# Kernel optimization log

Hardware: AMD Instinct MI355X
Metric: run time of the kernel (lower is better)

The kernel has to match this reference:

```python
import math
import jax, jax.numpy as jnp
import numpy as np

SIZE = 512
N_HEADS = 8
HEAD = SIZE // N_HEADS
SCALE = 1.0 / math.sqrt(HEAD)


def setup_inputs() -> dict:
    key = jax.random.key(0)
    ks = jax.random.split(key, 10)
    B, Sq, Skv = 4, 2048, 2048
    std = 1.0 / math.sqrt(SIZE)
    inp = {
        "query": jax.random.normal(ks[0], (B, Sq, SIZE), jnp.float32),
        "key_value": jax.random.normal(ks[1], (B, Skv, SIZE), jnp.float32),
        "Wq": jax.random.normal(ks[2], (SIZE, SIZE), jnp.float32) * std,
        "bq": jax.random.normal(ks[3], (SIZE,), jnp.float32) * std,
        "Wk": jax.random.normal(ks[4], (SIZE, SIZE), jnp.float32) * std,
        "bk": jax.random.normal(ks[5], (SIZE,), jnp.float32) * std,
        "Wv": jax.random.normal(ks[6], (SIZE, SIZE), jnp.float32) * std,
        "bv": jax.random.normal(ks[7], (SIZE,), jnp.float32) * std,
        "Wo": jax.random.normal(ks[8], (SIZE, SIZE), jnp.float32) * std,
        "bo": jax.random.normal(ks[9], (SIZE,), jnp.float32) * std,
    }
    return inp


def reference(query, key_value, Wq, bq, Wk, bk, Wv, bv, Wo, bo):
    B, Sq, D = query.shape
    Skv = key_value.shape[1]
    H, hd = N_HEADS, HEAD

    # Linear projections (torch nn.Linear: x @ W.T + b)
    q = query @ Wq.T + bq            # [B, Sq, D]
    k = key_value @ Wk.T + bk        # [B, Skv, D]
    v = key_value @ Wv.T + bv        # [B, Skv, D]

    # split heads: [B, S, H, hd]
    qh = q.reshape(B, Sq, H, hd)
    kh = k.reshape(B, Skv, H, hd)
    vh = v.reshape(B, Skv, H, hd)

    # attention scores and softmax over keys
    scores = jnp.einsum("bqhd,bkhd->bhqk", qh, kh) * SCALE  # [B, H, Sq, Skv]
    A = jax.nn.softmax(scores, axis=-1)
    o = jnp.einsum("bhqk,bkhd->bqhd", A, vh)                 # [B, Sq, H, hd]

    # residual with q heads (clean_path=False), merge heads
    out = (qh + o).reshape(B, Sq, D)

    # output residual + ReLU FFN stage
    out = out + jax.nn.relu(out @ Wo.T + bo)
    return out
```

## Files before the change

kernel.cpp:

```cpp
#include <hip/hip_runtime.h>
#include <hip/hip_bf16.h>

typedef __hip_bfloat16 bf16;
typedef __attribute__((ext_vector_type(4))) float f32x4;
typedef __attribute__((ext_vector_type(16))) float f32x16;
typedef __attribute__((ext_vector_type(8))) __bf16 bf16x8;

#define DEVI static __device__ __forceinline__

DEVI void gload_lds16(const void* g, void* l) {
  __builtin_amdgcn_global_load_lds(
      (const __attribute__((address_space(1))) void*)g,
      (__attribute__((address_space(3))) void*)l, 16, 0, 0);
}

DEVI unsigned pkbf(float a, float b) {
  union { __hip_bfloat162 h2; unsigned u; } t;
  t.h2.x = __float2bfloat16(a);
  t.h2.y = __float2bfloat16(b);
  return t.u;
}

union PK4 { bf16 h[4]; unsigned long long ll; };

DEVI unsigned long long pack4(float4 v) {
  PK4 u;
  u.h[0] = __float2bfloat16(v.x); u.h[1] = __float2bfloat16(v.y);
  u.h[2] = __float2bfloat16(v.z); u.h[3] = __float2bfloat16(v.w);
  return u.ll;
}

__global__ void cvt_all(const float* __restrict__ q, const float* __restrict__ kv,
                        const float* __restrict__ wq, const float* __restrict__ wk,
                        const float* __restrict__ wv, const float* __restrict__ wo,
                        bf16* __restrict__ oq, bf16* __restrict__ okv,
                        bf16* __restrict__ owq, bf16* __restrict__ owk,
                        bf16* __restrict__ owv, bf16* __restrict__ owo) {
  int bid = blockIdx.x;
  if (bid < 4096) {
    int i = bid * 256 + threadIdx.x;
    reinterpret_cast<unsigned long long*>(oq)[i]  = pack4(reinterpret_cast<const float4*>(q)[i]);
    reinterpret_cast<unsigned long long*>(okv)[i] = pack4(reinterpret_cast<const float4*>(kv)[i]);
  } else {
    int i = (bid - 4096) * 256 + threadIdx.x;
    reinterpret_cast<unsigned long long*>(owq)[i] = pack4(reinterpret_cast<const float4*>(wq)[i]);
    reinterpret_cast<unsigned long long*>(owk)[i] = pack4(reinterpret_cast<const float4*>(wk)[i]);
    reinterpret_cast<unsigned long long*>(owv)[i] = pack4(reinterpret_cast<const float4*>(wv)[i]);
    reinterpret_cast<unsigned long long*>(owo)[i] = pack4(reinterpret_cast<const float4*>(wo)[i]);
  }
}

__global__ __launch_bounds__(256) void gemm_qkv(
    const bf16* __restrict__ qb, const bf16* __restrict__ kvb,
    const bf16* __restrict__ wqb, const bf16* __restrict__ wkb, const bf16* __restrict__ wvb,
    const float* __restrict__ bq, const float* __restrict__ bk, const float* __restrict__ bv,
    bf16* __restrict__ qp, bf16* __restrict__ kp, bf16* __restrict__ vT) {
  constexpr int K = 512;
  __shared__ __align__(16) char smem[65536];
  const int tid = threadIdx.x;
  const int wave = tid >> 6, lane = tid & 63;
  const int bm = blockIdx.x;
  const int zone = blockIdx.y >> 2, bn = blockIdx.y & 3;
  const bf16* A = zone ? kvb : qb;
  const bf16* W = (zone == 0) ? wqb : (zone == 1 ? wkb : wvb);
  const float* bias = (zone == 0) ? bq : (zone == 1 ? bk : bv);
  const int wm = (wave >> 1) * 64, wn = (wave & 1) * 64;
  const int srow8 = lane >> 3, sslot = lane & 7;

  f32x4 acc[4][4] = {};

  const bf16* ap[4];
  const bf16* wp[4];
  char* adst[4];
  char* bdst[4];
#pragma unroll
  for (int i = 0; i < 4; ++i) {
    int c = wave * 4 + i;
    int row = c * 8 + srow8;
    int gs = sslot ^ (row & 7);
    ap[i] = A + (long)(bm * 128 + row) * K + gs * 8;
    wp[i] = W + (long)(bn * 128 + row) * K + gs * 8;
    adst[i] = smem + c * 1024;
    bdst[i] = smem + 16384 + c * 1024;
  }

  int aoff[2][4], boff[2][4];
#pragma unroll
  for (int ks = 0; ks < 2; ++ks)
#pragma unroll
    for (int f = 0; f < 4; ++f) {
      int r = f * 16 + (lane & 15);
      int sw = ((ks * 4 + (lane >> 4)) ^ (r & 7)) << 4;
      aoff[ks][f] = (wm + r) * 128 + sw;
      boff[ks][f] = (wn + r) * 128 + sw;
    }

#define GSTAGE(BUF)                                                       \
  _Pragma("unroll") for (int i = 0; i < 4; ++i) {                         \
    gload_lds16(ap[i], adst[i] + (BUF) * 32768);                          \
    gload_lds16(wp[i], bdst[i] + (BUF) * 32768);                          \
    ap[i] += 64; wp[i] += 64;                                             \
  }

#define GBODY(BUF, LAST)                                                  \
  {                                                                       \
    if (!(LAST)) {                                                        \
      GSTAGE((BUF) ^ 1)                                                   \
      asm volatile("s_waitcnt vmcnt(8)" ::: "memory");                    \
    } else {                                                              \
      asm volatile("s_waitcnt vmcnt(0)" ::: "memory");                    \
    }                                                                     \
    asm volatile("s_barrier" ::: "memory");                               \
    const char* Asb = smem + (BUF) * 32768;                               \
    const char* Bsb = Asb + 16384;                                        \
    _Pragma("unroll") for (int ks = 0; ks < 2; ++ks) {                    \
      bf16x8 af[4], bfv[4];                                               \
      _Pragma("unroll") for (int f = 0; f < 4; ++f) {                     \
        af[f]  = *reinterpret_cast<const bf16x8*>(Asb + aoff[ks][f]);     \
        bfv[f] = *reinterpret_cast<const bf16x8*>(Bsb + boff[ks][f]);     \
      }                                                                   \
      _Pragma("unroll") for (int mf = 0; mf < 4; ++mf)                    \
        _Pragma("unroll") for (int nf = 0; nf < 4; ++nf)                  \
          acc[mf][nf] = __builtin_amdgcn_mfma_f32_16x16x32_bf16(          \
              af[mf], bfv[nf], acc[mf][nf], 0, 0, 0);                     \
    }                                                                     \
    asm volatile("s_barrier" ::: "memory");                               \
  }

  GSTAGE(0)
#pragma unroll 1
  for (int kt = 0; kt < 8; kt += 2) {
    GBODY(0, false)
    GBODY(1, kt + 1 == 7)
  }
#undef GSTAGE
#undef GBODY

#pragma unroll
  for (int nf = 0; nf < 4; ++nf) {
    int col = bn * 128 + wn + nf * 16 + (lane & 15);
    float bia = bias[col];
#pragma unroll
    for (int mf = 0; mf < 4; ++mf) {
      int row0 = bm * 128 + wm + mf * 16 + (lane >> 4) * 4;
      if (zone < 2) {
        bf16* Ob = zone ? kp : qp;
#pragma unroll
        for (int j = 0; j < 4; ++j)
          Ob[(long)(row0 + j) * 512 + col] = __float2bfloat16(acc[mf][nf][j] + bia);
      } else {
        int b = row0 >> 11, s0 = row0 & 2047;
        int h = col >> 6, d = col & 63;
        union { ushort4 s; unsigned short u[4]; } pk;
#pragma unroll
        for (int j = 0; j < 4; ++j) {
          bf16 hv = __float2bfloat16(acc[mf][nf][j] + bia);
          pk.u[j] = *reinterpret_cast<unsigned short*>(&hv);
        }
        *reinterpret_cast<ushort4*>(vT + ((long)((b * 8 + h) * 64 + d)) * 2048 + s0) = pk.s;
      }
    }
  }
}

__global__ __launch_bounds__(256) void gemm_ffn(
    const bf16* __restrict__ A, const bf16* __restrict__ W,
    const float* __restrict__ bias, float* __restrict__ Of) {
  constexpr int K = 512;
  __shared__ __align__(16) char smem[49152];
  const int tid = threadIdx.x;
  const int wave = tid >> 6, lane = tid & 63;
  const int bm = blockIdx.x, bn = blockIdx.y;
  const int wm = (wave >> 1) * 32, wn = (wave & 1) * 64;
  const int srow8 = lane >> 3, sslot = lane & 7;

  f32x4 acc[2][4] = {};

  const bf16* ap[2];
  const bf16* wp[4];
  char* adst[2];
  char* bdst[4];
#pragma unroll
  for (int i = 0; i < 2; ++i) {
    int c = wave * 2 + i;
    int row = c * 8 + srow8;
    int gs = sslot ^ (row & 7);
    ap[i] = A + (long)(bm * 64 + row) * K + gs * 8;
    adst[i] = smem + c * 1024;
  }
#pragma unroll
  for (int i = 0; i < 4; ++i) {
    int c = wave * 4 + i;
    int row = c * 8 + srow8;
    int gs = sslot ^ (row & 7);
    wp[i] = W + (long)(bn * 128 + row) * K + gs * 8;
    bdst[i] = smem + 8192 + c * 1024;
  }

  int aoff[2][2], boff[2][4];
#pragma unroll
  for (int ks = 0; ks < 2; ++ks) {
#pragma unroll
    for (int f = 0; f < 2; ++f) {
      int r = f * 16 + (lane & 15);
      aoff[ks][f] = (wm + r) * 128 + (((ks * 4 + (lane >> 4)) ^ (r & 7)) << 4);
    }
#pragma unroll
    for (int f = 0; f < 4; ++f) {
      int r = f * 16 + (lane & 15);
      boff[ks][f] = (wn + r) * 128 + (((ks * 4 + (lane >> 4)) ^ (r & 7)) << 4);
    }
  }

#define FSTAGE(BUF)                                                       \
  {                                                                       \
    _Pragma("unroll") for (int i = 0; i < 2; ++i) {                       \
      gload_lds16(ap[i], adst[i] + (BUF) * 24576);                        \
      ap[i] += 64;                                                        \
    }                                                                     \
    _Pragma("unroll") for (int i = 0; i < 4; ++i) {                       \
      gload_lds16(wp[i], bdst[i] + (BUF) * 24576);                        \
      wp[i] += 64;                                                        \
    }                                                                     \
  }

#define FBODY(BUF, LAST)                                                  \
  {                                                                       \
    if (!(LAST)) {                                                        \
      FSTAGE((BUF) ^ 1)                                                   \
      asm volatile("s_waitcnt vmcnt(6)" ::: "memory");                    \
    } else {                                                              \
      asm volatile("s_waitcnt vmcnt(0)" ::: "memory");                    \
    }                                                                     \
    asm volatile("s_barrier" ::: "memory");                               \
    const char* Asb = smem + (BUF) * 24576;                               \
    const char* Bsb = Asb + 8192;                                         \
    _Pragma("unroll") for (int ks = 0; ks < 2; ++ks) {                    \
      bf16x8 af[2], bfv[4];                                               \
      _Pragma("unroll") for (int f = 0; f < 2; ++f)                       \
        af[f] = *reinterpret_cast<const bf16x8*>(Asb + aoff[ks][f]);      \
      _Pragma("unroll") for (int f = 0; f < 4; ++f)                       \
        bfv[f] = *reinterpret_cast<const bf16x8*>(Bsb + boff[ks][f]);     \
      _Pragma("unroll") for (int mf = 0; mf < 2; ++mf)                    \
        _Pragma("unroll") for (int nf = 0; nf < 4; ++nf)                  \
          acc[mf][nf] = __builtin_amdgcn_mfma_f32_16x16x32_bf16(          \
              af[mf], bfv[nf], acc[mf][nf], 0, 0, 0);                     \
    }                                                                     \
    asm volatile("s_barrier" ::: "memory");                               \
  }

  FSTAGE(0)
#pragma unroll 1
  for (int kt = 0; kt < 8; kt += 2) {
    FBODY(0, false)
    FBODY(1, kt + 1 == 7)
  }
#undef FSTAGE
#undef FBODY

#pragma unroll
  for (int nf = 0; nf < 4; ++nf) {
    int col = bn * 128 + wn + nf * 16 + (lane & 15);
    float bia = bias[col];
#pragma unroll
    for (int mf = 0; mf < 2; ++mf) {
#pragma unroll
      for (int j = 0; j < 4; ++j) {
        int row = bm * 64 + wm + mf * 16 + (lane >> 4) * 4 + j;
        float r = __bfloat162float(A[(long)row * 512 + col]);
        Of[(long)row * 512 + col] = r + fmaxf(acc[mf][nf][j] + bia, 0.f);
      }
    }
  }
}

__global__ __launch_bounds__(256) void attn_k(
    const bf16* __restrict__ Q, const bf16* __restrict__ Kp,
    const bf16* __restrict__ VT, bf16* __restrict__ O) {
  __shared__ __align__(16) char smem[32768];
  const int tid = threadIdx.x, wave = tid >> 6, lane = tid & 63;
  const int bh = blockIdx.y, b = bh >> 3, h = bh & 7;
  const int q0 = blockIdx.x * 128 + wave * 32;
  const int ql = lane & 31, hl = lane >> 5;
  const long qg = ((long)(b * 2048 + q0 + ql)) * 512 + h * 64;
  const int srow8 = lane >> 3, sslot = lane & 7;

  bf16x8 qf[4];
#pragma unroll
  for (int c = 0; c < 4; ++c)
    qf[c] = *reinterpret_cast<const bf16x8*>(Q + qg + c * 16 + hl * 8);

  bf16x8 ones;
#pragma unroll
  for (int j = 0; j < 8; ++j) ones[j] = (__bf16)1.0f;

  f32x16 oacc[2] = {};
  f32x16 lacc = {};
  float m = -INFINITY;
  const float CEXP = 0.125f * 1.44269504088896f;

  const bf16* kgp[2];
  const bf16* vgp[2];
  char* kdst[2];
  char* vdst[2];
#pragma unroll
  for (int i = 0; i < 2; ++i) {
    int c = wave * 2 + i;
    int row = c * 8 + srow8;
    int gs = sslot ^ (row & 7);
    kgp[i] = Kp + ((long)(b * 2048 + row)) * 512 + h * 64 + gs * 8;
    vgp[i] = VT + ((long)(bh * 64 + row)) * 2048 + gs * 8;
    kdst[i] = smem + c * 1024;
    vdst[i] = smem + 8192 + c * 1024;
  }

  int ofs[2][4];
#pragma unroll
  for (int s = 0; s < 2; ++s)
#pragma unroll
    for (int c = 0; c < 4; ++c) {
      int row = s * 32 + ql;
      ofs[s][c] = row * 128 + (((c * 2 + hl) ^ (row & 7)) << 4);
    }

#define ASTAGE(BUF)                                                       \
  _Pragma("unroll") for (int i = 0; i < 2; ++i) {                         \
    gload_lds16(kgp[i], kdst[i] + (BUF) * 16384);                         \
    gload_lds16(vgp[i], vdst[i] + (BUF) * 16384);                         \
    kgp[i] += 32768; vgp[i] += 64;                                        \
  }

#define ABODY(BUF, LAST)                                                  \
  {                                                                       \
    if (!(LAST)) {                                                        \
      ASTAGE((BUF) ^ 1)                                                   \
      asm volatile("s_waitcnt vmcnt(4)" ::: "memory");                    \
    } else {                                                              \
      asm volatile("s_waitcnt vmcnt(0)" ::: "memory");                    \
    }                                                                     \
    asm volatile("s_barrier" ::: "memory");                               \
    const char* Kb = smem + (BUF) * 16384;                                \
    const char* Vb = Kb + 8192;                                           \
    f32x16 sacc[2] = {};                                                  \
    __builtin_amdgcn_s_setprio(1);                                        \
    _Pragma("unroll") for (int s = 0; s < 2; ++s)                         \
      _Pragma("unroll") for (int c = 0; c < 4; ++c) {                     \
        bf16x8 kf = *reinterpret_cast<const bf16x8*>(Kb + ofs[s][c]);     \
        sacc[s] = __builtin_amdgcn_mfma_f32_32x32x16_bf16(                \
            kf, qf[c], sacc[s], 0, 0, 0);                                 \
      }                                                                   \
    __builtin_amdgcn_s_setprio(0);                                        \
    float pmax = fmaxf(sacc[0][0], sacc[0][1]);                           \
    _Pragma("unroll") for (int i = 2; i < 16; i += 2)                     \
      pmax = fmaxf(fmaxf(pmax, sacc[0][i]), sacc[0][i + 1]);              \
    _Pragma("unroll") for (int i = 0; i < 16; i += 2)                     \
      pmax = fmaxf(fmaxf(pmax, sacc[1][i]), sacc[1][i + 1]);              \
    pmax = fmaxf(pmax, __shfl_xor(pmax, 32));                             \
    if (!__all(pmax - m <= 44.3614195558365f)) {                          \
      float mn = fmaxf(m, pmax);                                          \
      float al = exp2f((m - mn) * CEXP);                                  \
      m = mn;                                                             \
      _Pragma("unroll") for (int i = 0; i < 16; ++i) {                    \
        oacc[0][i] *= al; oacc[1][i] *= al; lacc[i] *= al;                \
      }                                                                   \
    }                                                                     \
    float nmC = -m * CEXP;                                                \
    float p[32];                                                          \
    _Pragma("unroll") for (int s = 0; s < 2; ++s)                         \
      _Pragma("unroll") for (int i = 0; i < 16; ++i)                      \
        p[s * 16 + i] = exp2f(fmaf(sacc[s][i], CEXP, nmC));               \
    __builtin_amdgcn_s_setprio(1);                                        \
    _Pragma("unroll") for (int s = 0; s < 2; ++s)                         \
      _Pragma("unroll") for (int jj = 0; jj < 2; ++jj) {                  \
        int base = s * 16 + jj * 8;                                       \
        unsigned w0 = pkbf(p[base + 0], p[base + 1]);                     \
        unsigned w1 = pkbf(p[base + 2], p[base + 3]);                     \
        unsigned w2 = pkbf(p[base + 4], p[base + 5]);                     \
        unsigned w3 = pkbf(p[base + 6], p[base + 7]);                     \
        asm("v_permlane32_swap_b32 %0, %1" : "+v"(w0), "+v"(w2));         \
        asm("v_permlane32_swap_b32 %0, %1" : "+v"(w1), "+v"(w3));         \
        union { unsigned u[4]; bf16x8 v; } pf;                            \
        pf.u[0] = w0; pf.u[1] = w1; pf.u[2] = w2; pf.u[3] = w3;           \
        lacc = __builtin_amdgcn_mfma_f32_32x32x16_bf16(                   \
            ones, pf.v, lacc, 0, 0, 0);                                   \
        int j = s * 2 + jj;                                               \
        _Pragma("unroll") for (int dblk = 0; dblk < 2; ++dblk) {          \
          bf16x8 vf = *reinterpret_cast<const bf16x8*>(Vb + ofs[dblk][j]);\
          oacc[dblk] = __builtin_amdgcn_mfma_f32_32x32x16_bf16(           \
              vf, pf.v, oacc[dblk], 0, 0, 0);                             \
        }                                                                 \
      }                                                                   \
    __builtin_amdgcn_s_setprio(0);                                        \
    asm volatile("s_barrier" ::: "memory");                               \
  }

  ASTAGE(0)
#pragma unroll 1
  for (int tt = 0; tt < 16; ++tt) {
    ABODY(0, false)
    ABODY(1, tt == 15)
  }
#undef ASTAGE
#undef ABODY

  float rl = 1.0f / lacc[0];
#pragma unroll
  for (int dblk = 0; dblk < 2; ++dblk) {
#pragma unroll
    for (int g = 0; g < 4; ++g) {
      int d0 = dblk * 32 + g * 8 + hl * 4;
      const long ga = qg + d0;
      union { ushort4 s; unsigned short u[4]; } qin, ov;
      qin.s = *reinterpret_cast<const ushort4*>(Q + ga);
#pragma unroll
      for (int i = 0; i < 4; ++i) {
        float qvf = __uint_as_float((unsigned)qin.u[i] << 16);
        float r = qvf + oacc[dblk][g * 4 + i] * rl;
        bf16 hb = __float2bfloat16(r);
        ov.u[i] = *reinterpret_cast<unsigned short*>(&hb);
      }
      *reinterpret_cast<ushort4*>(O + ga) = ov.s;
    }
  }
}

extern "C" void kernel_launch(void* const* d_in, const int* in_sizes, int n_in,
                              void* d_out, int out_size, void* d_ws, size_t ws_size,
                              hipStream_t stream) {
  const float* query = (const float*)d_in[0];
  const float* keyv  = (const float*)d_in[1];
  const float* Wq = (const float*)d_in[2];
  const float* bq = (const float*)d_in[3];
  const float* Wk = (const float*)d_in[4];
  const float* bk = (const float*)d_in[5];
  const float* Wv = (const float*)d_in[6];
  const float* bv = (const float*)d_in[7];
  const float* Wo = (const float*)d_in[8];
  const float* bo = (const float*)d_in[9];
  float* out = (float*)d_out;
  char* ws = (char*)d_ws;

  bf16* qb  = (bf16*)(ws + 0);
  bf16* kvb = (bf16*)(ws + 8388608);
  bf16* wqb = (bf16*)(ws + 16777216);
  bf16* wkb = (bf16*)(ws + 17301504);
  bf16* wvb = (bf16*)(ws + 17825792);
  bf16* wob = (bf16*)(ws + 18350080);
  bf16* qp  = (bf16*)(ws + 18874368);
  bf16* kp  = (bf16*)(ws + 27262976);
  bf16* vT  = (bf16*)(ws + 35651584);
  bf16* o1  = (bf16*)(ws + 44040192);

  cvt_all<<<4352, 256, 0, stream>>>(query, keyv, Wq, Wk, Wv, Wo,
                                    qb, kvb, wqb, wkb, wvb, wob);

  gemm_qkv<<<dim3(64, 12), 256, 0, stream>>>(qb, kvb, wqb, wkb, wvb, bq, bk, bv, qp, kp, vT);

  attn_k<<<dim3(16, 32), 256, 0, stream>>>(qp, kp, vT, o1);

  gemm_ffn<<<dim3(128, 4), 256, 0, stream>>>(o1, wob, bo, out);
}
```

Before: 193.0 us.

## Split attention KV sequence across two wave groups and merge partial softmax

The attention kernel now launches 512 threads per block: two groups of four waves each process half of the 2048 keys for the same 128 queries, using separate LDS halves. At the end, the second group writes its partial output, max and sum to LDS, and the first group rescales and combines both results before writing. This doubles the waves available to hide latency with the same 512-block grid, at the cost of double the LDS per block, an extra merge step and a block-wide sync.

```diff
diff --git a/kernel.cpp b/kernel.cpp
--- a/kernel.cpp
+++ b/kernel.cpp
@@ -274,16 +274,18 @@
   }
 }
 
-__global__ __launch_bounds__(256) void attn_k(
+__global__ __launch_bounds__(512) void attn_k(
     const bf16* __restrict__ Q, const bf16* __restrict__ Kp,
     const bf16* __restrict__ VT, bf16* __restrict__ O) {
-  __shared__ __align__(16) char smem[32768];
+  __shared__ __align__(16) char smem[65536];
   const int tid = threadIdx.x, wave = tid >> 6, lane = tid & 63;
+  const int qwave = wave & 3, half = wave >> 2;
   const int bh = blockIdx.y, b = bh >> 3, h = bh & 7;
-  const int q0 = blockIdx.x * 128 + wave * 32;
+  const int q0 = blockIdx.x * 128 + qwave * 32;
   const int ql = lane & 31, hl = lane >> 5;
   const long qg = ((long)(b * 2048 + q0 + ql)) * 512 + h * 64;
   const int srow8 = lane >> 3, sslot = lane & 7;
+  char* hbase = smem + half * 32768;
 
   bf16x8 qf[4];
 #pragma unroll
@@ -305,13 +307,13 @@
   char* vdst[2];
 #pragma unroll
   for (int i = 0; i < 2; ++i) {
-    int c = wave * 2 + i;
+    int c = qwave * 2 + i;
     int row = c * 8 + srow8;
     int gs = sslot ^ (row & 7);
-    kgp[i] = Kp + ((long)(b * 2048 + row)) * 512 + h * 64 + gs * 8;
-    vgp[i] = VT + ((long)(bh * 64 + row)) * 2048 + gs * 8;
-    kdst[i] = smem + c * 1024;
-    vdst[i] = smem + 8192 + c * 1024;
+    kgp[i] = Kp + ((long)(b * 2048 + half * 1024 + row)) * 512 + h * 64 + gs * 8;
+    vgp[i] = VT + ((long)(bh * 64 + row)) * 2048 + half * 1024 + gs * 8;
+    kdst[i] = hbase + c * 1024;
+    vdst[i] = hbase + 8192 + c * 1024;
   }
 
   int ofs[2][4];
@@ -339,7 +341,7 @@
       asm volatile("s_waitcnt vmcnt(0)" ::: "memory");                    \
     }                                                                     \
     asm volatile("s_barrier" ::: "memory");                               \
-    const char* Kb = smem + (BUF) * 16384;                                \
+    const char* Kb = hbase + (BUF) * 16384;                               \
     const char* Vb = Kb + 8192;                                           \
     f32x16 sacc[2] = {};                                                  \
     __builtin_amdgcn_s_setprio(1);                                        \
@@ -396,30 +398,62 @@
 
   ASTAGE(0)
 #pragma unroll 1
-  for (int tt = 0; tt < 16; ++tt) {
+  for (int tt = 0; tt < 8; ++tt) {
     ABODY(0, false)
-    ABODY(1, tt == 15)
+    ABODY(1, tt == 7)
   }
 #undef ASTAGE
 #undef ABODY
 
-  float rl = 1.0f / lacc[0];
-#pragma unroll
-  for (int dblk = 0; dblk < 2; ++dblk) {
-#pragma unroll
-    for (int g = 0; g < 4; ++g) {
-      int d0 = dblk * 32 + g * 8 + hl * 4;
-      const long ga = qg + d0;
-      union { ushort4 s; unsigned short u[4]; } qin, ov;
-      qin.s = *reinterpret_cast<const ushort4*>(Q + ga);
-#pragma unroll
-      for (int i = 0; i < 4; ++i) {
-        float qvf = __uint_as_float((unsigned)qin.u[i] << 16);
-        float r = qvf + oacc[dblk][g * 4 + i] * rl;
-        bf16 hb = __float2bfloat16(r);
-        ov.u[i] = *reinterpret_cast<unsigned short*>(&hb);
+  char* qldsb = smem + qwave * 9216;
+  float* qldsf = reinterpret_cast<float*>(qldsb);
+
+  if (half == 1) {
+#pragma unroll
+    for (int dblk = 0; dblk < 2; ++dblk) {
+#pragma unroll
+      for (int g = 0; g < 4; ++g) {
+        int slot = dblk * 8 + g * 2 + hl;
+        f32x4 v;
+#pragma unroll
+        for (int i = 0; i < 4; ++i) v[i] = oacc[dblk][g * 4 + i];
+        *reinterpret_cast<f32x4*>(qldsb + ql * 256 + ((slot ^ (ql & 7)) << 4)) = v;
       }
-      *reinterpret_cast<ushort4*>(O + ga) = ov.s;
+    }
+    if (hl == 0) {
+      qldsf[2048 + ql] = m;
+      qldsf[2112 + ql] = lacc[0];
+    }
+  }
+  __syncthreads();
+
+  if (half == 0) {
+    float m1 = qldsf[2048 + ql];
+    float l1 = qldsf[2112 + ql];
+    float M = fmaxf(m, m1);
+    float e0 = exp2f((m - M) * CEXP);
+    float e1 = exp2f((m1 - M) * CEXP);
+    float L = lacc[0] * e0 + l1 * e1;
+    float rl = 1.0f / L;
+#pragma unroll
+    for (int dblk = 0; dblk < 2; ++dblk) {
+#pragma unroll
+      for (int g = 0; g < 4; ++g) {
+        int slot = dblk * 8 + g * 2 + hl;
+        f32x4 o1v = *reinterpret_cast<const f32x4*>(qldsb + ql * 256 + ((slot ^ (ql & 7)) << 4));
+        int d0 = dblk * 32 + g * 8 + hl * 4;
+        const long ga = qg + d0;
+        union { ushort4 s; unsigned short u[4]; } qin, ov;
+        qin.s = *reinterpret_cast<const ushort4*>(Q + ga);
+#pragma unroll
+        for (int i = 0; i < 4; ++i) {
+          float qvf = __uint_as_float((unsigned)qin.u[i] << 16);
+          float r = qvf + (oacc[dblk][g * 4 + i] * e0 + o1v[i] * e1) * rl;
+          bf16 hb = __float2bfloat16(r);
+          ov.u[i] = *reinterpret_cast<unsigned short*>(&hb);
+        }
+        *reinterpret_cast<ushort4*>(O + ga) = ov.s;
+      }
     }
   }
 }
@@ -456,7 +490,7 @@
 
   gemm_qkv<<<dim3(64, 12), 256, 0, stream>>>(qb, kvb, wqb, wkb, wvb, bq, bk, bv, qp, kp, vT);
 
-  attn_k<<<dim3(16, 32), 256, 0, stream>>>(qp, kp, vT, o1);
+  attn_k<<<dim3(16, 32), 512, 0, stream>>>(qp, kp, vT, o1);
 
   gemm_ffn<<<dim3(128, 4), 256, 0, stream>>>(o1, wob, bo, out);
 }
```

After: 198.6 us. 2.9% more time.

## Stage GEMM epilogues through swizzled LDS for coalesced stores; remap attention grid to XCDs

Applied to the files above, without the earlier changes.

The QKV and FFN GEMM epilogues now write accumulators into XOR-swizzled shared memory, then re-read them row-wise so each thread issues wide, coalesced global stores. This covers both the bf16 row-major outputs and the transposed V layout, and the FFN residual read is vectorized as well. Previously the epilogues did scattered 2-byte or 4-byte strided stores. The attention launch becomes a 1D grid with a block-index permutation, so consecutive blocks of the same head land on the same XCD and share L2. The cost is an extra LDS round trip and a barrier per tile.

```diff
diff --git a/kernel.cpp b/kernel.cpp
--- a/kernel.cpp
+++ b/kernel.cpp
@@ -5,6 +5,7 @@
 typedef __attribute__((ext_vector_type(4))) float f32x4;
 typedef __attribute__((ext_vector_type(16))) float f32x16;
 typedef __attribute__((ext_vector_type(8))) __bf16 bf16x8;
+typedef __attribute__((ext_vector_type(8))) unsigned short u16x8;
 
 #define DEVI static __device__ __forceinline__
 
@@ -19,6 +20,15 @@
   t.h2.x = __float2bfloat16(a);
   t.h2.y = __float2bfloat16(b);
   return t.u;
+}
+
+DEVI u16x8 cvt8(f32x4 a, f32x4 b) {
+  u16x8 r;
+#pragma unroll
+  for (int i = 0; i < 4; ++i) { bf16 h = __float2bfloat16(a[i]); r[i] = *reinterpret_cast<unsigned short*>(&h); }
+#pragma unroll
+  for (int i = 0; i < 4; ++i) { bf16 h = __float2bfloat16(b[i]); r[i + 4] = *reinterpret_cast<unsigned short*>(&h); }
+  return r;
 }
 
 union PK4 { bf16 h[4]; unsigned long long ll; };
@@ -138,26 +148,53 @@
 
 #pragma unroll
   for (int nf = 0; nf < 4; ++nf) {
-    int col = bn * 128 + wn + nf * 16 + (lane & 15);
-    float bia = bias[col];
-#pragma unroll
-    for (int mf = 0; mf < 4; ++mf) {
-      int row0 = bm * 128 + wm + mf * 16 + (lane >> 4) * 4;
-      if (zone < 2) {
-        bf16* Ob = zone ? kp : qp;
-#pragma unroll
-        for (int j = 0; j < 4; ++j)
-          Ob[(long)(row0 + j) * 512 + col] = __float2bfloat16(acc[mf][nf][j] + bia);
-      } else {
-        int b = row0 >> 11, s0 = row0 & 2047;
-        int h = col >> 6, d = col & 63;
-        union { ushort4 s; unsigned short u[4]; } pk;
+    int cl = wn + nf * 16 + (lane & 15);
+    float bia = bias[bn * 128 + cl];
+    if (zone < 2) {
+#pragma unroll
+      for (int mf = 0; mf < 4; ++mf) {
 #pragma unroll
         for (int j = 0; j < 4; ++j) {
-          bf16 hv = __float2bfloat16(acc[mf][nf][j] + bia);
-          pk.u[j] = *reinterpret_cast<unsigned short*>(&hv);
+          int r = wm + mf * 16 + (lane >> 4) * 4 + j;
+          *reinterpret_cast<float*>(smem + r * 512 + ((cl * 4) ^ ((r & 7) << 4))) =
+              acc[mf][nf][j] + bia;
         }
-        *reinterpret_cast<ushort4*>(vT + ((long)((b * 8 + h) * 64 + d)) * 2048 + s0) = pk.s;
+      }
+    } else {
+#pragma unroll
+      for (int mf = 0; mf < 4; ++mf) {
+        int r0 = wm + mf * 16 + (lane >> 4) * 4;
+        f32x4 v;
+#pragma unroll
+        for (int j = 0; j < 4; ++j) v[j] = acc[mf][nf][j] + bia;
+        *reinterpret_cast<f32x4*>(smem + cl * 512 + ((r0 * 4) ^ ((cl & 7) << 4))) = v;
+      }
+    }
+  }
+  __syncthreads();
+  {
+    int r = tid >> 1, half = tid & 1;
+    if (zone < 2) {
+      bf16* Ob = zone ? kp : qp;
+      long gbase = (long)(bm * 128 + r) * 512 + bn * 128 + half * 64;
+#pragma unroll
+      for (int k = 0; k < 8; ++k) {
+        int c0 = half * 64 + k * 8;
+        f32x4 a  = *reinterpret_cast<const f32x4*>(smem + r * 512 + ((c0 * 4) ^ ((r & 7) << 4)));
+        f32x4 b2 = *reinterpret_cast<const f32x4*>(smem + r * 512 + (((c0 + 4) * 4) ^ ((r & 7) << 4)));
+        *reinterpret_cast<u16x8*>(Ob + gbase + k * 8) = cvt8(a, b2);
+      }
+    } else {
+      int gcol = bn * 128 + r;
+      int hh = gcol >> 6, d = gcol & 63;
+      int b0 = bm >> 4;
+      long gbase = ((long)((b0 * 8 + hh) * 64 + d)) * 2048 + (bm & 15) * 128 + half * 64;
+#pragma unroll
+      for (int k = 0; k < 8; ++k) {
+        int r0 = half * 64 + k * 8;
+        f32x4 a  = *reinterpret_cast<const f32x4*>(smem + r * 512 + ((r0 * 4) ^ ((r & 7) << 4)));
+        f32x4 b2 = *reinterpret_cast<const f32x4*>(smem + r * 512 + (((r0 + 4) * 4) ^ ((r & 7) << 4)));
+        *reinterpret_cast<u16x8*>(vT + gbase + k * 8) = cvt8(a, b2);
       }
     }
   }
@@ -260,16 +297,35 @@
 
 #pragma unroll
   for (int nf = 0; nf < 4; ++nf) {
-    int col = bn * 128 + wn + nf * 16 + (lane & 15);
-    float bia = bias[col];
+    int cl = wn + nf * 16 + (lane & 15);
+    float bia = bias[bn * 128 + cl];
 #pragma unroll
     for (int mf = 0; mf < 2; ++mf) {
 #pragma unroll
       for (int j = 0; j < 4; ++j) {
-        int row = bm * 64 + wm + mf * 16 + (lane >> 4) * 4 + j;
-        float r = __bfloat162float(A[(long)row * 512 + col]);
-        Of[(long)row * 512 + col] = r + fmaxf(acc[mf][nf][j] + bia, 0.f);
-      }
+        int r = wm + mf * 16 + (lane >> 4) * 4 + j;
+        *reinterpret_cast<float*>(smem + r * 512 + ((cl * 4) ^ ((r & 7) << 4))) =
+            acc[mf][nf][j] + bia;
+      }
+    }
+  }
+  __syncthreads();
+  {
+    int r = tid >> 2, q = tid & 3;
+    long grow = (long)(bm * 64 + r) * 512 + bn * 128 + q * 32;
+#pragma unroll
+    for (int k = 0; k < 8; ++k) {
+      int c0 = q * 32 + k * 4;
+      f32x4 v = *reinterpret_cast<const f32x4*>(smem + r * 512 + ((c0 * 4) ^ ((r & 7) << 4)));
+      union { ushort4 s; unsigned short u[4]; } rin;
+      rin.s = *reinterpret_cast<const ushort4*>(A + grow + k * 4);
+      f32x4 o;
+#pragma unroll
+      for (int i = 0; i < 4; ++i) {
+        float rv = __uint_as_float((unsigned)rin.u[i] << 16);
+        o[i] = rv + fmaxf(v[i], 0.f);
+      }
+      *reinterpret_cast<f32x4*>(Of + grow + k * 4) = o;
     }
   }
 }
@@ -279,8 +335,11 @@
     const bf16* __restrict__ VT, bf16* __restrict__ O) {
   __shared__ __align__(16) char smem[32768];
   const int tid = threadIdx.x, wave = tid >> 6, lane = tid & 63;
-  const int bh = blockIdx.y, b = bh >> 3, h = bh & 7;
-  const int q0 = blockIdx.x * 128 + wave * 32;
+  const int bid = blockIdx.x;
+  const int f = (bid & 7) * 64 + (bid >> 3);
+  const int bh = f >> 4, qi = f & 15;
+  const int b = bh >> 3, h = bh & 7;
+  const int q0 = qi * 128 + wave * 32;
   const int ql = lane & 31, hl = lane >> 5;
   const long qg = ((long)(b * 2048 + q0 + ql)) * 512 + h * 64;
   const int srow8 = lane >> 3, sslot = lane & 7;
@@ -456,7 +515,7 @@
 
   gemm_qkv<<<dim3(64, 12), 256, 0, stream>>>(qb, kvb, wqb, wkb, wvb, bq, bk, bv, qp, kp, vT);
 
-  attn_k<<<dim3(16, 32), 256, 0, stream>>>(qp, kp, vT, o1);
+  attn_k<<<512, 256, 0, stream>>>(qp, kp, vT, o1);
 
   gemm_ffn<<<dim3(128, 4), 256, 0, stream>>>(o1, wob, bo, out);
 }
```

Result: slower. 205.3 us (+6.4%).

## Shrink QKV GEMM tile to 64 rows and remap workgroups for XCD locality

Applied to the files above, without the earlier changes.

Cuts the QKV projection GEMM block tile from 128x128 to 64x128, doubling the grid to 1536 workgroups and lowering LDS use to 48KB so more blocks can be resident. Both the QKV and FFN GEMMs now launch a 1D grid and remap block ids so that consecutive tiles sharing A rows land on the same XCD, which should improve L2 reuse. The smaller tile reads the weight tiles more often from memory and does less MFMA work per LDS load.

```diff
diff --git a/kernel.cpp b/kernel.cpp
--- a/kernel.cpp
+++ b/kernel.cpp
@@ -50,76 +50,94 @@
   }
 }
 
-__global__ __launch_bounds__(256) void gemm_qkv(
+__global__ __launch_bounds__(256) void gemm_zone(
     const bf16* __restrict__ qb, const bf16* __restrict__ kvb,
     const bf16* __restrict__ wqb, const bf16* __restrict__ wkb, const bf16* __restrict__ wvb,
     const float* __restrict__ bq, const float* __restrict__ bk, const float* __restrict__ bv,
     bf16* __restrict__ qp, bf16* __restrict__ kp, bf16* __restrict__ vT) {
   constexpr int K = 512;
-  __shared__ __align__(16) char smem[65536];
+  __shared__ __align__(16) char smem[49152];
   const int tid = threadIdx.x;
   const int wave = tid >> 6, lane = tid & 63;
-  const int bm = blockIdx.x;
-  const int zone = blockIdx.y >> 2, bn = blockIdx.y & 3;
+  const int bid = blockIdx.x;
+  const int wgid = (bid & 7) * 192 + (bid >> 3);
+  const int bm = wgid / 12;
+  const int rz = wgid % 12;
+  const int zone = rz >> 2, bn = rz & 3;
   const bf16* A = zone ? kvb : qb;
   const bf16* W = (zone == 0) ? wqb : (zone == 1 ? wkb : wvb);
   const float* bias = (zone == 0) ? bq : (zone == 1 ? bk : bv);
-  const int wm = (wave >> 1) * 64, wn = (wave & 1) * 64;
+  const int wm = (wave >> 1) * 32, wn = (wave & 1) * 64;
   const int srow8 = lane >> 3, sslot = lane & 7;
 
-  f32x4 acc[4][4] = {};
-
-  const bf16* ap[4];
+  f32x4 acc[2][4] = {};
+
+  const bf16* ap[2];
   const bf16* wp[4];
-  char* adst[4];
+  char* adst[2];
   char* bdst[4];
+#pragma unroll
+  for (int i = 0; i < 2; ++i) {
+    int c = wave * 2 + i;
+    int row = c * 8 + srow8;
+    int gs = sslot ^ (row & 7);
+    ap[i] = A + (long)(bm * 64 + row) * K + gs * 8;
+    adst[i] = smem + c * 1024;
+  }
 #pragma unroll
   for (int i = 0; i < 4; ++i) {
     int c = wave * 4 + i;
     int row = c * 8 + srow8;
     int gs = sslot ^ (row & 7);
-    ap[i] = A + (long)(bm * 128 + row) * K + gs * 8;
     wp[i] = W + (long)(bn * 128 + row) * K + gs * 8;
-    adst[i] = smem + c * 1024;
-    bdst[i] = smem + 16384 + c * 1024;
-  }
-
-  int aoff[2][4], boff[2][4];
-#pragma unroll
-  for (int ks = 0; ks < 2; ++ks)
+    bdst[i] = smem + 8192 + c * 1024;
+  }
+
+  int aoff[2][2], boff[2][4];
+#pragma unroll
+  for (int ks = 0; ks < 2; ++ks) {
+#pragma unroll
+    for (int f = 0; f < 2; ++f) {
+      int r = f * 16 + (lane & 15);
+      aoff[ks][f] = (wm + r) * 128 + (((ks * 4 + (lane >> 4)) ^ (r & 7)) << 4);
+    }
 #pragma unroll
     for (int f = 0; f < 4; ++f) {
       int r = f * 16 + (lane & 15);
-      int sw = ((ks * 4 + (lane >> 4)) ^ (r & 7)) << 4;
-      aoff[ks][f] = (wm + r) * 128 + sw;
-      boff[ks][f] = (wn + r) * 128 + sw;
-    }
-
-#define GSTAGE(BUF)                                                       \
-  _Pragma("unroll") for (int i = 0; i < 4; ++i) {                         \
-    gload_lds16(ap[i], adst[i] + (BUF) * 32768);                          \
-    gload_lds16(wp[i], bdst[i] + (BUF) * 32768);                          \
-    ap[i] += 64; wp[i] += 64;                                             \
-  }
-
-#define GBODY(BUF, LAST)                                                  \
+      boff[ks][f] = (wn + r) * 128 + (((ks * 4 + (lane >> 4)) ^ (r & 7)) << 4);
+    }
+  }
+
+#define ZSTAGE(BUF)                                                       \
+  {                                                                       \
+    _Pragma("unroll") for (int i = 0; i < 2; ++i) {                       \
+      gload_lds16(ap[i], adst[i] + (BUF) * 24576);                        \
+      ap[i] += 64;                                                        \
+    }                                                                     \
+    _Pragma("unroll") for (int i = 0; i < 4; ++i) {                       \
+      gload_lds16(wp[i], bdst[i] + (BUF) * 24576);                        \
+      wp[i] += 64;                                                        \
+    }                                                                     \
+  }
+
+#define ZBODY(BUF, LAST)                                                  \
   {                                                                       \
     if (!(LAST)) {                                                        \
-      GSTAGE((BUF) ^ 1)                                                   \
-      asm volatile("s_waitcnt vmcnt(8)" ::: "memory");                    \
+      ZSTAGE((BUF) ^ 1)                                                   \
+      asm volatile("s_waitcnt vmcnt(6)" ::: "memory");                    \
     } else {                                                              \
       asm volatile("s_waitcnt vmcnt(0)" ::: "memory");                    \
     }                                                                     \
     asm volatile("s_barrier" ::: "memory");                               \
-    const char* Asb = smem + (BUF) * 32768;                               \
-    const char* Bsb = Asb + 16384;                                        \
+    const char* Asb = smem + (BUF) * 24576;                               \
+    const char* Bsb = Asb + 8192;                                         \
     _Pragma("unroll") for (int ks = 0; ks < 2; ++ks) {                    \
-      bf16x8 af[4], bfv[4];                                               \
-      _Pragma("unroll") for (int f = 0; f < 4; ++f) {                     \
-        af[f]  = *reinterpret_cast<const bf16x8*>(Asb + aoff[ks][f]);     \
+      bf16x8 af[2], bfv[4];                                               \
+      _Pragma("unroll") for (int f = 0; f < 2; ++f)                       \
+        af[f] = *reinterpret_cast<const bf16x8*>(Asb + aoff[ks][f]);      \
+      _Pragma("unroll") for (int f = 0; f < 4; ++f)                       \
         bfv[f] = *reinterpret_cast<const bf16x8*>(Bsb + boff[ks][f]);     \
-      }                                                                   \
-      _Pragma("unroll") for (int mf = 0; mf < 4; ++mf)                    \
+      _Pragma("unroll") for (int mf = 0; mf < 2; ++mf)                    \
         _Pragma("unroll") for (int nf = 0; nf < 4; ++nf)                  \
           acc[mf][nf] = __builtin_amdgcn_mfma_f32_16x16x32_bf16(          \
               af[mf], bfv[nf], acc[mf][nf], 0, 0, 0);                     \
@@ -127,22 +145,22 @@
     asm volatile("s_barrier" ::: "memory");                               \
   }
 
-  GSTAGE(0)
+  ZSTAGE(0)
 #pragma unroll 1
   for (int kt = 0; kt < 8; kt += 2) {
-    GBODY(0, false)
-    GBODY(1, kt + 1 == 7)
-  }
-#undef GSTAGE
-#undef GBODY
+    ZBODY(0, false)
+    ZBODY(1, kt + 1 == 7)
+  }
+#undef ZSTAGE
+#undef ZBODY
 
 #pragma unroll
   for (int nf = 0; nf < 4; ++nf) {
     int col = bn * 128 + wn + nf * 16 + (lane & 15);
     float bia = bias[col];
 #pragma unroll
-    for (int mf = 0; mf < 4; ++mf) {
-      int row0 = bm * 128 + wm + mf * 16 + (lane >> 4) * 4;
+    for (int mf = 0; mf < 2; ++mf) {
+      int row0 = bm * 64 + wm + mf * 16 + (lane >> 4) * 4;
       if (zone < 2) {
         bf16* Ob = zone ? kp : qp;
 #pragma unroll
@@ -170,7 +188,9 @@
   __shared__ __align__(16) char smem[49152];
   const int tid = threadIdx.x;
   const int wave = tid >> 6, lane = tid & 63;
-  const int bm = blockIdx.x, bn = blockIdx.y;
+  const int bid = blockIdx.x;
+  const int wgid = (bid & 7) * 64 + (bid >> 3);
+  const int bm = wgid >> 2, bn = wgid & 3;
   const int wm = (wave >> 1) * 32, wn = (wave & 1) * 64;
   const int srow8 = lane >> 3, sslot = lane & 7;
 
@@ -454,9 +474,9 @@
   cvt_all<<<4352, 256, 0, stream>>>(query, keyv, Wq, Wk, Wv, Wo,
                                     qb, kvb, wqb, wkb, wvb, wob);
 
-  gemm_qkv<<<dim3(64, 12), 256, 0, stream>>>(qb, kvb, wqb, wkb, wvb, bq, bk, bv, qp, kp, vT);
+  gemm_zone<<<1536, 256, 0, stream>>>(qb, kvb, wqb, wkb, wvb, bq, bk, bv, qp, kp, vT);
 
   attn_k<<<dim3(16, 32), 256, 0, stream>>>(qp, kp, vT, o1);
 
-  gemm_ffn<<<dim3(128, 4), 256, 0, stream>>>(o1, wob, bo, out);
-}
+  gemm_ffn<<<512, 256, 0, stream>>>(o1, wob, bo, out);
+}
```

Result: no change. 194.4 us (+0.8%).
